# Optimization experiments

Hardware: AMD Instinct MI355X
Metric: run time of the kernel (lower is better)

## Reference

```python
import jax, jax.numpy as jnp
import numpy as np

N, E, F, H, G, C = 50000, 800000, 768, 256, 512, 2  # H = nhid*2 (nhid=128), G graphs, C classes
NHID = 128


def setup_inputs() -> dict:
    key = jax.random.key(0)
    ks = jax.random.split(key, 18)
    s = 0.05
    x = jax.random.normal(ks[0], (N, F), jnp.float32)
    edge_index = jax.random.randint(ks[1], (2, E), 0, N, dtype=jnp.int32)
    # sorted batch vector; every graph non-empty so the 'first node per graph' gather is valid
    batch = ((jnp.arange(N) * G) // N).astype(jnp.int32)
    return {
        "x": x,
        "edge_index": edge_index,
        "batch": batch,
        # GATConv 1 (in=F, out=H, heads=1)
        "W1": jax.random.normal(ks[2], (F, H), jnp.float32) * s,
        "as1": jax.random.normal(ks[3], (H,), jnp.float32) * s,
        "ad1": jax.random.normal(ks[4], (H,), jnp.float32) * s,
        "b1": jnp.zeros((H,), jnp.float32),
        # GATConv 2 (in=H, out=H)
        "W2": jax.random.normal(ks[5], (H, H), jnp.float32) * s,
        "as2": jax.random.normal(ks[6], (H,), jnp.float32) * s,
        "ad2": jax.random.normal(ks[7], (H,), jnp.float32) * s,
        "b2": jnp.zeros((H,), jnp.float32),
        # fc0: num_features -> nhid (news branch)
        "W0": jax.random.normal(ks[8], (F, NHID), jnp.float32) * s,
        "b0": jnp.zeros((NHID,), jnp.float32),
        # fc1: 2*nhid -> nhid (used twice, as in the source)
        "Wf1": jax.random.normal(ks[9], (H, NHID), jnp.float32) * s,
        "bf1": jnp.zeros((NHID,), jnp.float32),
        # fc2: nhid -> num_classes
        "Wf2": jax.random.normal(ks[10], (NHID, C), jnp.float32) * s,
        "bf2": jnp.zeros((C,), jnp.float32),
    }


def _gat(x, src, dst, W, a_s, a_d, b):
    # PyG GATConv, heads=1, concat=True, negative_slope=0.2, self-loops pre-appended to src/dst.
    h = x @ W                                   # [N, H]
    e = jax.nn.leaky_relu((h @ a_s)[src] + (h @ a_d)[dst], 0.2)  # [E+N]
    m = jax.ops.segment_max(e, dst, num_segments=N)
    ex = jnp.exp(e - m[dst])                    # stable segment softmax numerator
    denom = jax.ops.segment_sum(ex, dst, num_segments=N)
    agg = jax.ops.segment_sum(ex[:, None] * h[src], dst, num_segments=N)  # [N, H]
    return agg / denom[:, None] + b


def reference(x, edge_index, batch, W1, as1, ad1, b1, W2, as2, ad2, b2, W0, b0, Wf1, bf1, Wf2, bf2):
    loop = jnp.arange(N, dtype=edge_index.dtype)
    src = jnp.concatenate([edge_index[0], loop])  # add self-loops (PyG default)
    dst = jnp.concatenate([edge_index[1], loop])
    h = jax.nn.selu(_gat(x, src, dst, W1, as1, ad1, b1))
    h = jax.nn.selu(_gat(h, src, dst, W2, as2, ad2, b2))
    # global mean pool over graphs
    cnt = jax.ops.segment_sum(jnp.ones((N,), h.dtype), batch, num_segments=G)
    pooled = jax.nn.selu(jax.ops.segment_sum(h, batch, num_segments=G) / cnt[:, None])
    z = jax.nn.selu(pooled @ Wf1 + bf1)
    # dropout(p=0.5) in eval mode -> identity
    # concat branch: first node of each graph (news root)
    first_idx = jax.ops.segment_min(jnp.arange(N), batch, num_segments=G)
    news = jax.nn.relu(x[first_idx] @ W0 + b0)
    z = jnp.concatenate([z, news], axis=1)       # [G, 2*nhid]
    z = jax.nn.relu(z @ Wf1 + bf1)
    return jax.nn.log_softmax(z @ Wf2 + bf2, axis=-1)
```

## Files before the change

kernel.cpp:

```cpp
#include <hip/hip_runtime.h>
#include <hip/hip_bf16.h>
#include <cstdint>
#include <cstddef>

#define NN 50000
#define EE 800000
#define FF 768
#define HH 256
#define GG 512
#define CC 2
#define NHIDD 128
#define ETOT (EE + NN)
#define NCHUNK 49

typedef __attribute__((ext_vector_type(8))) short bf16x8;
typedef __attribute__((ext_vector_type(4))) float f32x4;
typedef __attribute__((ext_vector_type(8))) unsigned short us8;

__device__ __forceinline__ float b2f(unsigned short u){
  union { float f; uint32_t i; } v; v.i = ((uint32_t)u) << 16; return v.f;
}
__device__ __forceinline__ unsigned short f2b(float f){
  uint32_t u = __float_as_uint(f);
  uint32_t r = (u + 0x7fffu + ((u >> 16) & 1u)) >> 16;
  return (unsigned short)r;
}
__device__ __forceinline__ float selu_f(float x){
  const float lam = 1.0507009873554805f, alp = 1.6732632423543772f;
  return x > 0.f ? lam * x : lam * alp * (__expf(x) - 1.f);
}

__global__ __launch_bounds__(256) void swizzleW(const float* __restrict__ W,
                                                unsigned short* __restrict__ Wsw, int K){
  int i = blockIdx.x * 256 + threadIdx.x;
  if (i < K * HH){
    int k = i / HH, n = i % HH;
    Wsw[(size_t)(k >> 5) * 8192 + n * 32 + (k & 31)] = f2b(W[i]);
  }
}

__global__ __launch_bounds__(256) void zero_deg(int* deg){
  int i = blockIdx.x * 256 + threadIdx.x;
  if (i < NN) deg[i] = 0;
}

__global__ __launch_bounds__(256) void deg_kernel(const int* __restrict__ dstA, int* __restrict__ deg){
  int i = blockIdx.x * 256 + threadIdx.x;
  if (i < ETOT){
    int d = (i < EE) ? dstA[i] : (i - EE);
    atomicAdd(&deg[d], 1);
  }
}

__global__ __launch_bounds__(256) void scanA(const int* __restrict__ deg, int* __restrict__ bsum){
  __shared__ int red[256];
  int c = blockIdx.x, tid = threadIdx.x;
  int base = c * 1024 + tid * 4;
  int s = 0;
#pragma unroll
  for (int j = 0; j < 4; j++){ int idx = base + j; if (idx < NN) s += deg[idx]; }
  red[tid] = s; __syncthreads();
  for (int off = 128; off > 0; off >>= 1){
    if (tid < off) red[tid] += red[tid + off];
    __syncthreads();
  }
  if (tid == 0) bsum[c] = red[0];
}

__global__ void scanB(int* bsum){
  if (threadIdx.x == 0){
    int run = 0;
    for (int i = 0; i < NCHUNK; i++){ int v = bsum[i]; bsum[i] = run; run += v; }
  }
}

__global__ __launch_bounds__(256) void scanC(const int* __restrict__ deg, const int* __restrict__ bsum,
                                             int* __restrict__ row_ptr, int* __restrict__ fill_ptr){
  __shared__ int ts[256];
  int c = blockIdx.x, tid = threadIdx.x;
  int base = c * 1024 + tid * 4;
  int v[4]; int s = 0;
#pragma unroll
  for (int j = 0; j < 4; j++){ int idx = base + j; v[j] = (idx < NN) ? deg[idx] : 0; s += v[j]; }
  ts[tid] = s; __syncthreads();
  for (int off = 1; off < 256; off <<= 1){
    int add = (tid >= off) ? ts[tid - off] : 0;
    __syncthreads();
    ts[tid] += add;
    __syncthreads();
  }
  int run = ts[tid] - s + bsum[c];
#pragma unroll
  for (int j = 0; j < 4; j++){
    int idx = base + j;
    if (idx < NN){ row_ptr[idx] = run; fill_ptr[idx] = run; }
    run += v[j];
  }
  if (c == 0 && tid == 0) row_ptr[NN] = ETOT;
}

__global__ __launch_bounds__(256) void fill_kernel(const int* __restrict__ srcA, const int* __restrict__ dstA,
                                                   int* __restrict__ fill_ptr, int* __restrict__ csr_src){
  int i = blockIdx.x * 256 + threadIdx.x;
  if (i < ETOT){
    int s = (i < EE) ? srcA[i] : (i - EE);
    int d = (i < EE) ? dstA[i] : (i - EE);
    int pos = atomicAdd(&fill_ptr[d], 1);
    csr_src[pos] = s;
  }
}

template<int K, bool AF32>
__global__ __launch_bounds__(256) void gemm_mfma(const void* __restrict__ Ap,
                                                 const unsigned short* __restrict__ Wsw,
                                                 unsigned short* __restrict__ out, int M){
  __shared__ unsigned short Al[2][64][40];
  const int tid = threadIdx.x;
  const int m0 = blockIdx.x * 64;
  const int lane = tid & 63, w = tid >> 6;
  const int koff = (lane >> 4) * 8;
  const int arow = lane & 15;
  const int nrow = w * 64 + (lane & 15);
  const int srow = tid >> 2, skc = (tid & 3) * 8;
  const bool rowok = (m0 + srow < M);

  f32x4 acc[4][4];
#pragma unroll
  for (int rt = 0; rt < 4; rt++)
#pragma unroll
    for (int ct = 0; ct < 4; ct++) acc[rt][ct] = (f32x4){0.f, 0.f, 0.f, 0.f};

  auto stageA = [&](int ks, int buf){
    if (rowok){
      if (AF32){
        const float* Af = (const float*)Ap;
        size_t ab = (size_t)(m0 + srow) * K + ks * 32 + skc;
        float4 f0 = *(const float4*)&Af[ab];
        float4 f1 = *(const float4*)&Af[ab + 4];
        us8 v;
        v[0] = f2b(f0.x); v[1] = f2b(f0.y); v[2] = f2b(f0.z); v[3] = f2b(f0.w);
        v[4] = f2b(f1.x); v[5] = f2b(f1.y); v[6] = f2b(f1.z); v[7] = f2b(f1.w);
        *(us8*)&Al[buf][srow][skc] = v;
      } else {
        const unsigned short* Au = (const unsigned short*)Ap;
        *(us8*)&Al[buf][srow][skc] = *(const us8*)&Au[(size_t)(m0 + srow) * K + ks * 32 + skc];
      }
    } else {
      us8 z = {0,0,0,0,0,0,0,0}; *(us8*)&Al[buf][srow][skc] = z;
    }
  };

  constexpr int NIT = K / 32;
  stageA(0, 0);
  bf16x8 bcur[4];
  {
    const unsigned short* bp = Wsw + ((size_t)nrow * 32 + koff);
#pragma unroll
    for (int ct = 0; ct < 4; ct++) bcur[ct] = *(const bf16x8*)(bp + ct * 512);
  }
  __syncthreads();

  for (int ks = 0; ks < NIT; ks++){
    bf16x8 bnext[4];
    if (ks + 1 < NIT){
      const unsigned short* bp = Wsw + ((size_t)(ks + 1) * 8192 + (size_t)nrow * 32 + koff);
#pragma unroll
      for (int ct = 0; ct < 4; ct++) bnext[ct] = *(const bf16x8*)(bp + ct * 512);
      stageA(ks + 1, (ks + 1) & 1);
    }
    bf16x8 af[4];
#pragma unroll
    for (int rt = 0; rt < 4; rt++) af[rt] = *(const bf16x8*)&Al[ks & 1][rt * 16 + arow][koff];
#pragma unroll
    for (int rt = 0; rt < 4; rt++)
#pragma unroll
      for (int ct = 0; ct < 4; ct++)
        acc[rt][ct] = __builtin_amdgcn_mfma_f32_16x16x32_bf16(af[rt], bcur[ct], acc[rt][ct], 0, 0, 0);
    if (ks + 1 < NIT){
#pragma unroll
      for (int ct = 0; ct < 4; ct++) bcur[ct] = bnext[ct];
    }
    __syncthreads();
  }

#pragma unroll
  for (int rt = 0; rt < 4; rt++){
    int mbase = m0 + rt * 16 + (lane >> 4) * 4;
#pragma unroll
    for (int r = 0; r < 4; r++){
      int m = mbase + r;
      if (m < M){
        size_t ro = (size_t)m * HH + w * 64 + (lane & 15);
        out[ro + 0]  = f2b(acc[rt][0][r]);
        out[ro + 16] = f2b(acc[rt][1][r]);
        out[ro + 32] = f2b(acc[rt][2][r]);
        out[ro + 48] = f2b(acc[rt][3][r]);
      }
    }
  }
}

__global__ __launch_bounds__(256) void alsald_kernel(const unsigned short* __restrict__ h,
    const float* __restrict__ a_s, const float* __restrict__ a_d,
    float* __restrict__ als, float* __restrict__ ald){
  int node = blockIdx.x * 4 + (threadIdx.x >> 6);
  int lane = threadIdx.x & 63;
  if (node >= NN) return;
  ushort4 hv = *(const ushort4*)&h[(size_t)node * HH + lane * 4];
  float4 as4 = *(const float4*)&a_s[lane * 4];
  float4 ad4 = *(const float4*)&a_d[lane * 4];
  float h0 = b2f(hv.x), h1 = b2f(hv.y), h2 = b2f(hv.z), h3 = b2f(hv.w);
  float s = h0 * as4.x + h1 * as4.y + h2 * as4.z + h3 * as4.w;
  float d = h0 * ad4.x + h1 * ad4.y + h2 * ad4.z + h3 * ad4.w;
  for (int off = 32; off > 0; off >>= 1){ s += __shfl_xor(s, off); d += __shfl_xor(d, off); }
  if (lane == 0){ als[node] = s; ald[node] = d; }
}

__global__ __launch_bounds__(256) void agg_wave(const unsigned short* __restrict__ h,
    const float* __restrict__ als, const float* __restrict__ ald,
    const int* __restrict__ row_ptr, const int* __restrict__ csr_src,
    const float* __restrict__ bias, unsigned short* __restrict__ outp){
  int node = blockIdx.x * 4 + (threadIdx.x >> 6);
  int lane = threadIdx.x & 63;
  if (node >= NN) return;
  int base = row_ptr[node];
  int deg  = row_ptr[node + 1] - base;
  float aldd = ald[node];
  float den = 0.f;
  float a0 = 0.f, a1 = 0.f, a2 = 0.f, a3 = 0.f;
  const size_t fo = (size_t)lane * 4;
  for (int p0 = 0; p0 < deg; p0 += 64){
    int cnt = min(64, deg - p0);
    float ev = 0.f; int s = 0;
    if (lane < cnt){
      s = csr_src[base + p0 + lane];
      float v = als[s] + aldd;
      v = v > 0.f ? v : 0.2f * v;
      ev = __expf(v);
    }
    den += ev;
    int j = 0;
    for (; j + 2 <= cnt; j += 2){
      float e0 = __shfl(ev, j), e1 = __shfl(ev, j + 1);
      int s0 = __shfl(s, j), s1 = __shfl(s, j + 1);
      ushort4 g0 = *(const ushort4*)&h[(size_t)s0 * HH + fo];
      ushort4 g1 = *(const ushort4*)&h[(size_t)s1 * HH + fo];
      a0 += e0 * b2f(g0.x) + e1 * b2f(g1.x);
      a1 += e0 * b2f(g0.y) + e1 * b2f(g1.y);
      a2 += e0 * b2f(g0.z) + e1 * b2f(g1.z);
      a3 += e0 * b2f(g0.w) + e1 * b2f(g1.w);
    }
    for (; j < cnt; j++){
      float e0 = __shfl(ev, j); int s0 = __shfl(s, j);
      ushort4 g0 = *(const ushort4*)&h[(size_t)s0 * HH + fo];
      a0 += e0 * b2f(g0.x); a1 += e0 * b2f(g0.y); a2 += e0 * b2f(g0.z); a3 += e0 * b2f(g0.w);
    }
  }
  for (int off = 32; off > 0; off >>= 1) den += __shfl_xor(den, off);
  float inv = 1.f / den;
  float4 b4 = *(const float4*)&bias[fo];
  ushort4 o;
  o.x = f2b(selu_f(a0 * inv + b4.x));
  o.y = f2b(selu_f(a1 * inv + b4.y));
  o.z = f2b(selu_f(a2 * inv + b4.z));
  o.w = f2b(selu_f(a3 * inv + b4.w));
  *(ushort4*)&outp[(size_t)node * HH + fo] = o;
}

__global__ __launch_bounds__(256) void first_kernel(const int* __restrict__ batch, int* __restrict__ first_idx){
  int n = blockIdx.x * 256 + threadIdx.x;
  if (n < NN){
    int b = batch[n];
    if (n == 0 || batch[n - 1] != b) first_idx[b] = n;
  }
  if (blockIdx.x == 0 && threadIdx.x == 0) first_idx[GG] = NN;
}

__global__ __launch_bounds__(256) void pool_kernel(const unsigned short* __restrict__ x3,
    const int* __restrict__ first_idx, float* __restrict__ pooled){
  int g = blockIdx.x, f = threadIdx.x;
  int s = first_idx[g], e = first_idx[g + 1];
  float acc = 0.f;
  for (int n = s; n < e; n++) acc += b2f(x3[(size_t)n * HH + f]);
  pooled[g * HH + f] = selu_f(acc / (float)(e - s));
}

__global__ __launch_bounds__(128) void z1_kernel(const float* __restrict__ pooled,
    const float* __restrict__ Wf1, const float* __restrict__ bf1,
    float* __restrict__ z1){
  __shared__ float pr[HH];
  int g = blockIdx.x, t = threadIdx.x;
  pr[t] = pooled[g * HH + t];
  pr[t + 128] = pooled[g * HH + t + 128];
  __syncthreads();
  float acc = 0.f;
  for (int k = 0; k < HH; k++) acc += pr[k] * Wf1[k * NHIDD + t];
  z1[g * NHIDD + t] = selu_f(acc + bf1[t]);
}

__global__ __launch_bounds__(128) void news_kernel(const float* __restrict__ x,
    const int* __restrict__ first_idx, const float* __restrict__ W0,
    const float* __restrict__ b0, float* __restrict__ znews){
  __shared__ float xr[FF];
  int g = blockIdx.x, t = threadIdx.x;
  int root = first_idx[g];
  for (int k = t; k < FF; k += 128) xr[k] = x[(size_t)root * FF + k];
  __syncthreads();
  float acc = 0.f;
  for (int k = 0; k < FF; k++) acc += xr[k] * W0[k * NHIDD + t];
  acc += b0[t];
  znews[g * NHIDD + t] = acc > 0.f ? acc : 0.f;
}

__global__ __launch_bounds__(128) void final_kernel(const float* __restrict__ z1,
    const float* __restrict__ znews, const float* __restrict__ Wf1,
    const float* __restrict__ bf1, const float* __restrict__ Wf2,
    const float* __restrict__ bf2, float* __restrict__ out){
  __shared__ float zc[HH];
  __shared__ float l0s[2], l1s[2];
  int g = blockIdx.x, t = threadIdx.x;
  zc[t] = z1[g * NHIDD + t];
  zc[NHIDD + t] = znews[g * NHIDD + t];
  __syncthreads();
  float acc = 0.f;
  for (int k = 0; k < HH; k++) acc += zc[k] * Wf1[k * NHIDD + t];
  float z2 = acc + bf1[t]; z2 = z2 > 0.f ? z2 : 0.f;
  float p0 = z2 * Wf2[t * CC + 0];
  float p1 = z2 * Wf2[t * CC + 1];
  for (int off = 32; off > 0; off >>= 1){ p0 += __shfl_xor(p0, off); p1 += __shfl_xor(p1, off); }
  int lane = t & 63, wid = t >> 6;
  if (lane == 0){ l0s[wid] = p0; l1s[wid] = p1; }
  __syncthreads();
  if (t == 0){
    float l0 = l0s[0] + l0s[1] + bf2[0];
    float l1 = l1s[0] + l1s[1] + bf2[1];
    float mx = fmaxf(l0, l1);
    float lse = mx + logf(__expf(l0 - mx) + __expf(l1 - mx));
    out[g * CC + 0] = l0 - lse;
    out[g * CC + 1] = l1 - lse;
  }
}

extern "C" void kernel_launch(void* const* d_in, const int* in_sizes, int n_in,
                              void* d_out, int out_size, void* d_ws, size_t ws_size,
                              hipStream_t stream){
  const float* x          = (const float*)d_in[0];
  const int* edge_index   = (const int*)d_in[1];
  const int* batch        = (const int*)d_in[2];
  const float* W1  = (const float*)d_in[3];
  const float* as1 = (const float*)d_in[4];
  const float* ad1 = (const float*)d_in[5];
  const float* b1  = (const float*)d_in[6];
  const float* W2  = (const float*)d_in[7];
  const float* as2 = (const float*)d_in[8];
  const float* ad2 = (const float*)d_in[9];
  const float* b2  = (const float*)d_in[10];
  const float* W0  = (const float*)d_in[11];
  const float* b0  = (const float*)d_in[12];
  const float* Wf1 = (const float*)d_in[13];
  const float* bf1 = (const float*)d_in[14];
  const float* Wf2 = (const float*)d_in[15];
  const float* bf2 = (const float*)d_in[16];
  float* out = (float*)d_out;

  char* w = (char*)d_ws;
  size_t off = 0;
  auto alloc = [&](size_t bytes){ size_t o = off; off += (bytes + 255) & ~(size_t)255; return o; };
  unsigned short* h    = (unsigned short*)(w + alloc((size_t)NN * HH * 2));
  unsigned short* x2   = (unsigned short*)(w + alloc((size_t)NN * HH * 2));
  unsigned short* Wsw1 = (unsigned short*)(w + alloc((size_t)FF * HH * 2));
  unsigned short* Wsw2 = (unsigned short*)(w + alloc((size_t)HH * HH * 2));
  float* als     = (float*)(w + alloc((size_t)NN * 4));
  float* ald     = (float*)(w + alloc((size_t)NN * 4));
  int*   deg     = (int*)(w + alloc((size_t)NN * 4));
  int*   row_ptr = (int*)(w + alloc((size_t)(NN + 1) * 4));
  int*   fillp   = (int*)(w + alloc((size_t)NN * 4));
  int*   csr_src = (int*)(w + alloc((size_t)ETOT * 4));
  int*   bsum    = (int*)(w + alloc(64 * 4));
  int*   firsti  = (int*)(w + alloc((size_t)(GG + 1) * 4));
  float* pooled  = (float*)(w + alloc((size_t)GG * HH * 4));
  float* z1      = (float*)(w + alloc((size_t)GG * NHIDD * 4));
  float* znews   = (float*)(w + alloc((size_t)GG * NHIDD * 4));

  const int* srcA = edge_index;
  const int* dstA = edge_index + EE;

  swizzleW<<<(FF * HH + 255) / 256, 256, 0, stream>>>(W1, Wsw1, FF);
  swizzleW<<<(HH * HH + 255) / 256, 256, 0, stream>>>(W2, Wsw2, HH);

  zero_deg<<<(NN + 255) / 256, 256, 0, stream>>>(deg);
  deg_kernel<<<(ETOT + 255) / 256, 256, 0, stream>>>(dstA, deg);
  scanA<<<NCHUNK, 256, 0, stream>>>(deg, bsum);
  scanB<<<1, 64, 0, stream>>>(bsum);
  scanC<<<NCHUNK, 256, 0, stream>>>(deg, bsum, row_ptr, fillp);
  fill_kernel<<<(ETOT + 255) / 256, 256, 0, stream>>>(srcA, dstA, fillp, csr_src);

  const int gemm_grid = (NN + 63) / 64;
  gemm_mfma<FF, true><<<gemm_grid, 256, 0, stream>>>((const void*)x, Wsw1, h, NN);
  alsald_kernel<<<(NN + 3) / 4, 256, 0, stream>>>(h, as1, ad1, als, ald);
  agg_wave<<<(NN + 3) / 4, 256, 0, stream>>>(h, als, ald, row_ptr, csr_src, b1, x2);
  gemm_mfma<HH, false><<<gemm_grid, 256, 0, stream>>>((const void*)x2, Wsw2, h, NN);
  alsald_kernel<<<(NN + 3) / 4, 256, 0, stream>>>(h, as2, ad2, als, ald);
  agg_wave<<<(NN + 3) / 4, 256, 0, stream>>>(h, als, ald, row_ptr, csr_src, b2, x2);
  first_kernel<<<(NN + 255) / 256, 256, 0, stream>>>(batch, firsti);
  pool_kernel<<<GG, 256, 0, stream>>>(x2, firsti, pooled);
  z1_kernel<<<GG, 128, 0, stream>>>(pooled, Wf1, bf1, z1);
  news_kernel<<<GG, 128, 0, stream>>>(x, firsti, W0, b0, znews);
  final_kernel<<<GG, 128, 0, stream>>>(z1, znews, Wf1, bf1, Wf2, bf2, out);
}
```

Measured before the change: 614.0 us.

## Halve GEMM M-tile to 32 rows and double K-step to 64

The MFMA GEMM tile changes from 64x256 to 32x256 with a K step of 64 instead of 32, staging a 32x64 A tile per iteration and prefetching two K-slices of swizzled W. This doubles the grid size and halves the number of K-loop iterations and barriers, with the aim of better occupancy and latency hiding. In exchange, each W fragment is reused by fewer rows, so W traffic from cache per output roughly doubles.

```diff
diff --git a/kernel.cpp b/kernel.cpp
--- a/kernel.cpp
+++ b/kernel.cpp
@@ -114,19 +114,19 @@
 __global__ __launch_bounds__(256) void gemm_mfma(const void* __restrict__ Ap,
                                                  const unsigned short* __restrict__ Wsw,
                                                  unsigned short* __restrict__ out, int M){
-  __shared__ unsigned short Al[2][64][40];
+  __shared__ unsigned short Al[2][32][72];
   const int tid = threadIdx.x;
-  const int m0 = blockIdx.x * 64;
+  const int m0 = blockIdx.x * 32;
   const int lane = tid & 63, w = tid >> 6;
   const int koff = (lane >> 4) * 8;
   const int arow = lane & 15;
   const int nrow = w * 64 + (lane & 15);
-  const int srow = tid >> 2, skc = (tid & 3) * 8;
+  const int srow = tid >> 3, skc = (tid & 7) * 8;
   const bool rowok = (m0 + srow < M);
 
-  f32x4 acc[4][4];
-#pragma unroll
-  for (int rt = 0; rt < 4; rt++)
+  f32x4 acc[2][4];
+#pragma unroll
+  for (int rt = 0; rt < 2; rt++)
 #pragma unroll
     for (int ct = 0; ct < 4; ct++) acc[rt][ct] = (f32x4){0.f, 0.f, 0.f, 0.f};
 
@@ -134,7 +134,7 @@
     if (rowok){
       if (AF32){
         const float* Af = (const float*)Ap;
-        size_t ab = (size_t)(m0 + srow) * K + ks * 32 + skc;
+        size_t ab = (size_t)(m0 + srow) * K + ks * 64 + skc;
         float4 f0 = *(const float4*)&Af[ab];
         float4 f1 = *(const float4*)&Af[ab + 4];
         us8 v;
@@ -143,48 +143,59 @@
         *(us8*)&Al[buf][srow][skc] = v;
       } else {
         const unsigned short* Au = (const unsigned short*)Ap;
-        *(us8*)&Al[buf][srow][skc] = *(const us8*)&Au[(size_t)(m0 + srow) * K + ks * 32 + skc];
+        *(us8*)&Al[buf][srow][skc] = *(const us8*)&Au[(size_t)(m0 + srow) * K + ks * 64 + skc];
       }
     } else {
       us8 z = {0,0,0,0,0,0,0,0}; *(us8*)&Al[buf][srow][skc] = z;
     }
   };
 
-  constexpr int NIT = K / 32;
+  constexpr int NIT = K / 64;
   stageA(0, 0);
-  bf16x8 bcur[4];
-  {
-    const unsigned short* bp = Wsw + ((size_t)nrow * 32 + koff);
-#pragma unroll
-    for (int ct = 0; ct < 4; ct++) bcur[ct] = *(const bf16x8*)(bp + ct * 512);
+  bf16x8 bcur[2][4];
+#pragma unroll
+  for (int k2 = 0; k2 < 2; k2++){
+    const unsigned short* bp = Wsw + ((size_t)k2 * 8192 + (size_t)nrow * 32 + koff);
+#pragma unroll
+    for (int ct = 0; ct < 4; ct++) bcur[k2][ct] = *(const bf16x8*)(bp + ct * 512);
   }
   __syncthreads();
 
   for (int ks = 0; ks < NIT; ks++){
-    bf16x8 bnext[4];
+    bf16x8 bnext[2][4];
     if (ks + 1 < NIT){
-      const unsigned short* bp = Wsw + ((size_t)(ks + 1) * 8192 + (size_t)nrow * 32 + koff);
-#pragma unroll
-      for (int ct = 0; ct < 4; ct++) bnext[ct] = *(const bf16x8*)(bp + ct * 512);
+#pragma unroll
+      for (int k2 = 0; k2 < 2; k2++){
+        const unsigned short* bp = Wsw + ((size_t)((ks + 1) * 2 + k2) * 8192 + (size_t)nrow * 32 + koff);
+#pragma unroll
+        for (int ct = 0; ct < 4; ct++) bnext[k2][ct] = *(const bf16x8*)(bp + ct * 512);
+      }
       stageA(ks + 1, (ks + 1) & 1);
     }
-    bf16x8 af[4];
-#pragma unroll
-    for (int rt = 0; rt < 4; rt++) af[rt] = *(const bf16x8*)&Al[ks & 1][rt * 16 + arow][koff];
-#pragma unroll
-    for (int rt = 0; rt < 4; rt++)
-#pragma unroll
-      for (int ct = 0; ct < 4; ct++)
-        acc[rt][ct] = __builtin_amdgcn_mfma_f32_16x16x32_bf16(af[rt], bcur[ct], acc[rt][ct], 0, 0, 0);
+    bf16x8 af[2][2];
+#pragma unroll
+    for (int k2 = 0; k2 < 2; k2++)
+#pragma unroll
+      for (int rt = 0; rt < 2; rt++)
+        af[k2][rt] = *(const bf16x8*)&Al[ks & 1][rt * 16 + arow][k2 * 32 + koff];
+#pragma unroll
+    for (int k2 = 0; k2 < 2; k2++)
+#pragma unroll
+      for (int rt = 0; rt < 2; rt++)
+#pragma unroll
+        for (int ct = 0; ct < 4; ct++)
+          acc[rt][ct] = __builtin_amdgcn_mfma_f32_16x16x32_bf16(af[k2][rt], bcur[k2][ct], acc[rt][ct], 0, 0, 0);
     if (ks + 1 < NIT){
 #pragma unroll
-      for (int ct = 0; ct < 4; ct++) bcur[ct] = bnext[ct];
+      for (int k2 = 0; k2 < 2; k2++)
+#pragma unroll
+        for (int ct = 0; ct < 4; ct++) bcur[k2][ct] = bnext[k2][ct];
     }
     __syncthreads();
   }
 
 #pragma unroll
-  for (int rt = 0; rt < 4; rt++){
+  for (int rt = 0; rt < 2; rt++){
     int mbase = m0 + rt * 16 + (lane >> 4) * 4;
 #pragma unroll
     for (int r = 0; r < 4; r++){
@@ -395,7 +406,7 @@
   scanC<<<NCHUNK, 256, 0, stream>>>(deg, bsum, row_ptr, fillp);
   fill_kernel<<<(ETOT + 255) / 256, 256, 0, stream>>>(srcA, dstA, fillp, csr_src);
 
-  const int gemm_grid = (NN + 63) / 64;
+  const int gemm_grid = (NN + 31) / 32;
   gemm_mfma<FF, true><<<gemm_grid, 256, 0, stream>>>((const void*)x, Wsw1, h, NN);
   alsald_kernel<<<(NN + 3) / 4, 256, 0, stream>>>(h, as1, ad1, als, ald);
   agg_wave<<<(NN + 3) / 4, 256, 0, stream>>>(h, als, ald, row_ptr, csr_src, b1, x2);
```

After: 605.4 us. No clear change (-1.4%).
